# Optimization experiments

Hardware: AMD Instinct MI355X
Metric: run time of the kernel (lower is better)

The kernel has to match this reference:

```python
import jax, jax.numpy as jnp
import numpy as np


def setup_inputs() -> dict:
    key = jax.random.key(0)
    k1, k2 = jax.random.split(key)
    B, Tc, Tq, D = 8, 2048, 1024, 1024
    similarity = jax.random.normal(k1, (B, Tc, Tq), dtype=jnp.float32)
    qencode = jax.random.normal(k2, (B, Tq, D), dtype=jnp.float32)
    return {"similarity": similarity, "qencode": qencode}


def reference(similarity, qencode):
    # softmax over query axis, then weighted sum of query encodings:
    # equivalent to softmax(similarity, -1) @ qencode, avoiding the
    # [B, Tc, Tq, D] broadcasted intermediate of the original TF code.
    attn = jax.nn.softmax(similarity, axis=-1)          # [B, Tc, Tq]
    c2q = jnp.einsum("bcq,bqd->bcd", attn, qencode)     # [B, Tc, D]
    return c2q
```

## Files before the change

### kernel.cpp

```cpp
#include <hip/hip_runtime.h>
#include <hip/hip_bf16.h>
#include <stdint.h>

#define BATCH 8
#define TC 2048
#define TQ 1024
#define DD 1024

typedef __attribute__((ext_vector_type(8))) __bf16 bf16x8;
typedef __attribute__((ext_vector_type(4))) float f32x4;
typedef __attribute__((ext_vector_type(8))) ushort ushort8v;

__device__ __forceinline__ ushort f2bf(float f) {
    uint32_t u = __float_as_uint(f);
    uint32_t r = (u + 0x7fffu + ((u >> 16) & 1u)) >> 16;
    return (ushort)r;
}

__global__ __launch_bounds__(256) void rowstats(const float* __restrict__ sim,
                                                float2* __restrict__ stats) {
    const int t = threadIdx.x;
    const int wid = t >> 6, lane = t & 63;
    const int r0 = blockIdx.x * 8 + wid * 2;

    const float4* s0 = (const float4*)(sim + (size_t)r0 * TQ);
    const float4* s1 = (const float4*)(sim + (size_t)(r0 + 1) * TQ);

    float4 x0[4], x1[4];
    #pragma unroll
    for (int j = 0; j < 4; j++) { x0[j] = s0[lane + 64 * j]; x1[j] = s1[lane + 64 * j]; }

    float m0 = -INFINITY, m1 = -INFINITY;
    #pragma unroll
    for (int j = 0; j < 4; j++) {
        m0 = fmaxf(m0, fmaxf(fmaxf(x0[j].x, x0[j].y), fmaxf(x0[j].z, x0[j].w)));
        m1 = fmaxf(m1, fmaxf(fmaxf(x1[j].x, x1[j].y), fmaxf(x1[j].z, x1[j].w)));
    }
    #pragma unroll
    for (int o = 32; o >= 1; o >>= 1) {
        m0 = fmaxf(m0, __shfl_xor(m0, o));
        m1 = fmaxf(m1, __shfl_xor(m1, o));
    }

    const float L2E = 1.4426950408889634f;
    float sa = 0.f, sb = 0.f;
    #pragma unroll
    for (int j = 0; j < 4; j++) {
        {
            float e0 = exp2f((x0[j].x - m0) * L2E);
            float e1 = exp2f((x0[j].y - m0) * L2E);
            float e2 = exp2f((x0[j].z - m0) * L2E);
            float e3 = exp2f((x0[j].w - m0) * L2E);
            sa += (e0 + e1) + (e2 + e3);
        }
        {
            float e0 = exp2f((x1[j].x - m1) * L2E);
            float e1 = exp2f((x1[j].y - m1) * L2E);
            float e2 = exp2f((x1[j].z - m1) * L2E);
            float e3 = exp2f((x1[j].w - m1) * L2E);
            sb += (e0 + e1) + (e2 + e3);
        }
    }
    #pragma unroll
    for (int o = 32; o >= 1; o >>= 1) {
        sa += __shfl_xor(sa, o);
        sb += __shfl_xor(sb, o);
    }

    if (lane == 0) {
        float4 out = make_float4(m0, 1.0f / sa, m1, 1.0f / sb);
        *(float4*)&stats[r0] = out;
    }
}

__global__ __launch_bounds__(256) void transp(const float* __restrict__ qen,
                                              ushort* __restrict__ qt) {
    __shared__ float tile[64][133];
    const int t = threadIdx.x;
    const int bid = blockIdx.x;
    const int b = bid >> 7;
    const int rem = bid & 127;
    const int q0 = (rem >> 3) * 64;
    const int d0 = (rem & 7) * 128;

    const int r0 = t >> 5;
    const int cf = (t & 31) * 4;

    float4 v[8];
    #pragma unroll
    for (int it = 0; it < 8; it++)
        v[it] = *(const float4*)(qen + ((size_t)b * TQ + q0 + r0 + it * 8) * DD + d0 + cf);
    #pragma unroll
    for (int it = 0; it < 8; it++) {
        tile[r0 + it * 8][cf + 0] = v[it].x;
        tile[r0 + it * 8][cf + 1] = v[it].y;
        tile[r0 + it * 8][cf + 2] = v[it].z;
        tile[r0 + it * 8][cf + 3] = v[it].w;
    }
    __syncthreads();

    const int q8 = (t & 7) * 8;
    const int dbase = t >> 3;
    #pragma unroll
    for (int j2 = 0; j2 < 4; j2++) {
        const int d = dbase + 32 * j2;
        ushort8v pk;
        #pragma unroll
        for (int j = 0; j < 8; j++) pk[j] = f2bf(tile[q8 + j][d]);
        *(ushort8v*)(qt + ((size_t)b * DD + d0 + d) * TQ + q0 + q8) = pk;
    }
}

__global__ __launch_bounds__(256, 2) void gemm_fused(const float* __restrict__ S,
                                                     const float2* __restrict__ st,
                                                     const ushort* __restrict__ Bt,
                                                     float* __restrict__ C) {
    __shared__ __align__(16) ushort As[128 * 64];
    __shared__ __align__(16) ushort Bs[128 * 64];

    const int flat = blockIdx.x;
    const int b = flat >> 7;
    const int rem = flat & 127;
    const int group = rem >> 5;
    const int mi_t = group * 4 + (rem & 3);
    const int ni_t = (rem >> 2) & 7;
    const int tm0 = mi_t * 128;
    const int tn0 = ni_t * 128;

    const float* Sb = S + (size_t)b * TC * TQ;
    const ushort* Bb = Bt + (size_t)b * DD * TQ;
    float* Cb = C + (size_t)b * TC * DD;

    const int t = threadIdx.x;
    const int w = t >> 6, lane = t & 63;
    const int quad = lane >> 4, l16 = lane & 15;
    const int wm = (w >> 1) * 64, wn = (w & 1) * 64;

    f32x4 acc[4][4];
    #pragma unroll
    for (int i = 0; i < 4; i++)
        #pragma unroll
        for (int j = 0; j < 4; j++) acc[i][j] = (f32x4){0.f, 0.f, 0.f, 0.f};

    const int srow = w * 8 + (lane >> 3);
    const int sk = ((lane & 7) ^ (lane >> 3)) * 8;
    const int rkey = l16 & 7;

    const float L2E = 1.4426950408889634f;

    float2 stv[4];
    #pragma unroll
    for (int i = 0; i < 4; i++)
        stv[i] = st[(size_t)b * TC + tm0 + i * 32 + srow];

    for (int kk = 0; kk < TQ; kk += 64) {
        float4 xa[4][2];
        #pragma unroll
        for (int i = 0; i < 4; i++) {
            const float* g = Sb + (size_t)(tm0 + i * 32 + srow) * TQ + kk + sk;
            xa[i][0] = *(const float4*)g;
            xa[i][1] = *(const float4*)(g + 4);
        }
        #pragma unroll
        for (int i = 0; i < 4; i++) {
            const ushort* gb = Bb + (size_t)(tn0 + i * 32 + srow) * TQ + kk + sk;
            char* lb = (char*)Bs + i * 4096 + w * 1024;
            __builtin_amdgcn_global_load_lds(
                (const __attribute__((address_space(1))) void*)gb,
                (__attribute__((address_space(3))) void*)lb, 16, 0, 0);
        }
        #pragma unroll
        for (int i = 0; i < 4; i++) {
            const float mm = stv[i].x, iv = stv[i].y;
            ushort8v pk;
            pk[0] = f2bf(exp2f((xa[i][0].x - mm) * L2E) * iv);
            pk[1] = f2bf(exp2f((xa[i][0].y - mm) * L2E) * iv);
            pk[2] = f2bf(exp2f((xa[i][0].z - mm) * L2E) * iv);
            pk[3] = f2bf(exp2f((xa[i][0].w - mm) * L2E) * iv);
            pk[4] = f2bf(exp2f((xa[i][1].x - mm) * L2E) * iv);
            pk[5] = f2bf(exp2f((xa[i][1].y - mm) * L2E) * iv);
            pk[6] = f2bf(exp2f((xa[i][1].z - mm) * L2E) * iv);
            pk[7] = f2bf(exp2f((xa[i][1].w - mm) * L2E) * iv);
            *(ushort8v*)&As[i * 2048 + w * 512 + lane * 8] = pk;
        }
        __syncthreads();

        #pragma unroll
        for (int s = 0; s < 2; s++) {
            const int rswz = ((s * 4 + quad) ^ rkey) * 8;
            bf16x8 af[4], bfr[4];
            #pragma unroll
            for (int mi = 0; mi < 4; mi++)
                af[mi] = *(const bf16x8*)&As[(wm + mi * 16 + l16) * 64 + rswz];
            #pragma unroll
            for (int ni = 0; ni < 4; ni++)
                bfr[ni] = *(const bf16x8*)&Bs[(wn + ni * 16 + l16) * 64 + rswz];

            #pragma unroll
            for (int mi = 0; mi < 4; mi++)
                #pragma unroll
                for (int ni = 0; ni < 4; ni++)
                    acc[mi][ni] = __builtin_amdgcn_mfma_f32_16x16x32_bf16(
                        af[mi], bfr[ni], acc[mi][ni], 0, 0, 0);
        }
        __syncthreads();
    }

    #pragma unroll
    for (int mi = 0; mi < 4; mi++) {
        const int r0 = tm0 + wm + mi * 16 + quad * 4;
        #pragma unroll
        for (int ni = 0; ni < 4; ni++) {
            const int c = tn0 + wn + ni * 16 + l16;
            f32x4 v = acc[mi][ni];
            #pragma unroll
            for (int r = 0; r < 4; r++) Cb[(size_t)(r0 + r) * DD + c] = v[r];
        }
    }
}

extern "C" void kernel_launch(void* const* d_in, const int* in_sizes, int n_in,
                              void* d_out, int out_size, void* d_ws, size_t ws_size,
                              hipStream_t stream) {
    const float* sim = (const float*)d_in[0];
    const float* qen = (const float*)d_in[1];
    float* out = (float*)d_out;

    ushort* qt = (ushort*)d_ws;
    float2* stats = (float2*)((char*)d_ws + (size_t)BATCH * DD * TQ * 2);

    rowstats<<<BATCH * TC / 8, 256, 0, stream>>>(sim, stats);
    transp<<<BATCH * (TQ / 64) * (DD / 128), 256, 0, stream>>>(qen, qt);
    gemm_fused<<<BATCH * (TC / 128) * (DD / 128), 256, 0, stream>>>(sim, stats, qt, out);
}
```

Measured before the change: 211.1 us.

## Materialize bf16 softmax in a prepass and use a pure bf16 GEMM

The row-stats kernel now writes the fully normalized softmax as bf16 into workspace, and the GEMM loads both operands straight into LDS with global_load_lds instead of re-reading fp32 similarity and recomputing exp per tile. This removes the repeated exp and fp32 A-tile traffic from each of the 8 column tiles, at the cost of an extra 32 MB bf16 write and read. The block-to-batch mapping is also interleaved so that consecutive blocks fall in different batches.

```diff
diff --git a/kernel.cpp b/kernel.cpp
--- a/kernel.cpp
+++ b/kernel.cpp
@@ -17,8 +17,8 @@
     return (ushort)r;
 }
 
-__global__ __launch_bounds__(256) void rowstats(const float* __restrict__ sim,
-                                                float2* __restrict__ stats) {
+__global__ __launch_bounds__(256) void softmax2(const float* __restrict__ sim,
+                                                ushort* __restrict__ attn) {
     const int t = threadIdx.x;
     const int wid = t >> 6, lane = t & 63;
     const int r0 = blockIdx.x * 8 + wid * 2;
@@ -46,30 +46,39 @@
     float sa = 0.f, sb = 0.f;
     #pragma unroll
     for (int j = 0; j < 4; j++) {
-        {
-            float e0 = exp2f((x0[j].x - m0) * L2E);
-            float e1 = exp2f((x0[j].y - m0) * L2E);
-            float e2 = exp2f((x0[j].z - m0) * L2E);
-            float e3 = exp2f((x0[j].w - m0) * L2E);
-            sa += (e0 + e1) + (e2 + e3);
-        }
-        {
-            float e0 = exp2f((x1[j].x - m1) * L2E);
-            float e1 = exp2f((x1[j].y - m1) * L2E);
-            float e2 = exp2f((x1[j].z - m1) * L2E);
-            float e3 = exp2f((x1[j].w - m1) * L2E);
-            sb += (e0 + e1) + (e2 + e3);
-        }
+        x0[j].x = exp2f((x0[j].x - m0) * L2E);
+        x0[j].y = exp2f((x0[j].y - m0) * L2E);
+        x0[j].z = exp2f((x0[j].z - m0) * L2E);
+        x0[j].w = exp2f((x0[j].w - m0) * L2E);
+        sa += (x0[j].x + x0[j].y) + (x0[j].z + x0[j].w);
+        x1[j].x = exp2f((x1[j].x - m1) * L2E);
+        x1[j].y = exp2f((x1[j].y - m1) * L2E);
+        x1[j].z = exp2f((x1[j].z - m1) * L2E);
+        x1[j].w = exp2f((x1[j].w - m1) * L2E);
+        sb += (x1[j].x + x1[j].y) + (x1[j].z + x1[j].w);
     }
     #pragma unroll
     for (int o = 32; o >= 1; o >>= 1) {
         sa += __shfl_xor(sa, o);
         sb += __shfl_xor(sb, o);
     }
-
-    if (lane == 0) {
-        float4 out = make_float4(m0, 1.0f / sa, m1, 1.0f / sb);
-        *(float4*)&stats[r0] = out;
+    const float iva = 1.0f / sa, ivb = 1.0f / sb;
+
+    ushort4* d0 = (ushort4*)(attn + (size_t)r0 * TQ);
+    ushort4* d1 = (ushort4*)(attn + (size_t)(r0 + 1) * TQ);
+    #pragma unroll
+    for (int j = 0; j < 4; j++) {
+        ushort4 o4;
+        o4.x = f2bf(x0[j].x * iva);
+        o4.y = f2bf(x0[j].y * iva);
+        o4.z = f2bf(x0[j].z * iva);
+        o4.w = f2bf(x0[j].w * iva);
+        d0[lane + 64 * j] = o4;
+        o4.x = f2bf(x1[j].x * ivb);
+        o4.y = f2bf(x1[j].y * ivb);
+        o4.z = f2bf(x1[j].z * ivb);
+        o4.w = f2bf(x1[j].w * ivb);
+        d1[lane + 64 * j] = o4;
     }
 }
 
@@ -111,23 +120,22 @@
     }
 }
 
-__global__ __launch_bounds__(256, 2) void gemm_fused(const float* __restrict__ S,
-                                                     const float2* __restrict__ st,
-                                                     const ushort* __restrict__ Bt,
-                                                     float* __restrict__ C) {
+__global__ __launch_bounds__(256, 2) void gemm_bf16(const ushort* __restrict__ A,
+                                                    const ushort* __restrict__ Bt,
+                                                    float* __restrict__ C) {
     __shared__ __align__(16) ushort As[128 * 64];
     __shared__ __align__(16) ushort Bs[128 * 64];
 
     const int flat = blockIdx.x;
-    const int b = flat >> 7;
-    const int rem = flat & 127;
+    const int b = flat & 7;
+    const int rem = flat >> 3;
     const int group = rem >> 5;
     const int mi_t = group * 4 + (rem & 3);
     const int ni_t = (rem >> 2) & 7;
     const int tm0 = mi_t * 128;
     const int tn0 = ni_t * 128;
 
-    const float* Sb = S + (size_t)b * TC * TQ;
+    const ushort* Ab = A + (size_t)b * TC * TQ;
     const ushort* Bb = Bt + (size_t)b * DD * TQ;
     float* Cb = C + (size_t)b * TC * DD;
 
@@ -144,44 +152,22 @@
 
     const int srow = w * 8 + (lane >> 3);
     const int sk = ((lane & 7) ^ (lane >> 3)) * 8;
+
     const int rkey = l16 & 7;
 
-    const float L2E = 1.4426950408889634f;
-
-    float2 stv[4];
-    #pragma unroll
-    for (int i = 0; i < 4; i++)
-        stv[i] = st[(size_t)b * TC + tm0 + i * 32 + srow];
-
     for (int kk = 0; kk < TQ; kk += 64) {
-        float4 xa[4][2];
         #pragma unroll
         for (int i = 0; i < 4; i++) {
-            const float* g = Sb + (size_t)(tm0 + i * 32 + srow) * TQ + kk + sk;
-            xa[i][0] = *(const float4*)g;
-            xa[i][1] = *(const float4*)(g + 4);
-        }
-        #pragma unroll
-        for (int i = 0; i < 4; i++) {
+            const ushort* ga = Ab + (size_t)(tm0 + i * 32 + srow) * TQ + kk + sk;
             const ushort* gb = Bb + (size_t)(tn0 + i * 32 + srow) * TQ + kk + sk;
+            char* la = (char*)As + i * 4096 + w * 1024;
             char* lb = (char*)Bs + i * 4096 + w * 1024;
+            __builtin_amdgcn_global_load_lds(
+                (const __attribute__((address_space(1))) void*)ga,
+                (__attribute__((address_space(3))) void*)la, 16, 0, 0);
             __builtin_amdgcn_global_load_lds(
                 (const __attribute__((address_space(1))) void*)gb,
                 (__attribute__((address_space(3))) void*)lb, 16, 0, 0);
-        }
-        #pragma unroll
-        for (int i = 0; i < 4; i++) {
-            const float mm = stv[i].x, iv = stv[i].y;
-            ushort8v pk;
-            pk[0] = f2bf(exp2f((xa[i][0].x - mm) * L2E) * iv);
-            pk[1] = f2bf(exp2f((xa[i][0].y - mm) * L2E) * iv);
-            pk[2] = f2bf(exp2f((xa[i][0].z - mm) * L2E) * iv);
-            pk[3] = f2bf(exp2f((xa[i][0].w - mm) * L2E) * iv);
-            pk[4] = f2bf(exp2f((xa[i][1].x - mm) * L2E) * iv);
-            pk[5] = f2bf(exp2f((xa[i][1].y - mm) * L2E) * iv);
-            pk[6] = f2bf(exp2f((xa[i][1].z - mm) * L2E) * iv);
-            pk[7] = f2bf(exp2f((xa[i][1].w - mm) * L2E) * iv);
-            *(ushort8v*)&As[i * 2048 + w * 512 + lane * 8] = pk;
         }
         __syncthreads();
 
@@ -226,10 +212,10 @@
     const float* qen = (const float*)d_in[1];
     float* out = (float*)d_out;
 
-    ushort* qt = (ushort*)d_ws;
-    float2* stats = (float2*)((char*)d_ws + (size_t)BATCH * DD * TQ * 2);
-
-    rowstats<<<BATCH * TC / 8, 256, 0, stream>>>(sim, stats);
+    ushort* attn = (ushort*)d_ws;
+    ushort* qt = (ushort*)d_ws + (size_t)BATCH * TC * TQ;
+
+    softmax2<<<BATCH * TC / 8, 256, 0, stream>>>(sim, attn);
     transp<<<BATCH * (TQ / 64) * (DD / 128), 256, 0, stream>>>(qen, qt);
-    gemm_fused<<<BATCH * (TC / 128) * (DD / 128), 256, 0, stream>>>(sim, stats, qt, out);
-}
+    gemm_bf16<<<BATCH * (TC / 128) * (DD / 128), 256, 0, stream>>>(attn, qt, out);
+}
```

Result: faster. 177.7 us (-15.8%).
